# Kernel optimization log

Measured on AMD Instinct MI355X. Metric: run time of the kernel, lower is better.

Reference implementation:

```python
import jax, jax.numpy as jnp
import numpy as np

N, E, D = 50000, 800000, 128   # nodes, edges, hidden dim (in_dim == out_dim == 128)
MSG_EPS = 1e-7                 # GENConv eps added to relu(msg)
SM_EPS = 1e-16                 # PyG softmax denominator eps


def _glorotish(key, shape, fan_in):
    return jax.random.normal(key, shape, jnp.float32) * (1.0 / np.sqrt(fan_in))


def setup_inputs() -> dict:
    key = jax.random.key(0)
    ks = jax.random.split(key, 8)
    return dict(
        x=jax.random.normal(ks[0], (N, D), jnp.float32),
        edge_index=jax.random.randint(ks[1], (2, E), 0, N),
        edge_attr=jax.random.uniform(ks[2], (E, 1), jnp.float32),
        # GENConv params (bias=False internals, per PyG defaults)
        W_edge=_glorotish(ks[3], (D, 1), 1),          # lin_edge: edge_dim=1 -> D
        t=jnp.array(1.0, jnp.float32),                # learnable softmax temperature
        W1=_glorotish(ks[4], (2 * D, D), D),          # MLP: D -> 2D
        bn_gamma=jnp.ones((2 * D,), jnp.float32),     # BatchNorm1d affine
        bn_beta=jnp.zeros((2 * D,), jnp.float32),
        W2=_glorotish(ks[5], (D, 2 * D), 2 * D),      # MLP: 2D -> D
        # outer LayerNorm
        ln_gamma=jnp.ones((D,), jnp.float32),
        ln_beta=jnp.zeros((D,), jnp.float32),
        # edge_mlp: Linear(2D -> D) + GELU + LayerNorm
        We=_glorotish(ks[6], (D, 2 * D), 2 * D),
        be=jnp.zeros((D,), jnp.float32),
        ln_e_gamma=jnp.ones((D,), jnp.float32),
        ln_e_beta=jnp.zeros((D,), jnp.float32),
    )


def layer_norm(x, g, b, eps=1e-5):
    mu = x.mean(-1, keepdims=True)
    var = x.var(-1, keepdims=True)
    return (x - mu) * jax.lax.rsqrt(var + eps) * g + b


def reference(x, edge_index, edge_attr, W_edge, t, W1, bn_gamma, bn_beta, W2,
              ln_gamma, ln_beta, We, be, ln_e_gamma, ln_e_beta):
    src, dst = edge_index[0], edge_index[1]

    # --- GENConv ---
    e = edge_attr @ W_edge.T                                  # [E, D] lin_edge
    msg = jax.nn.relu(x[src] + e) + MSG_EPS                   # [E, D] message

    # per-destination scatter-softmax (per channel), temperature t
    scores = msg * t
    smax = jax.ops.segment_max(scores, dst, num_segments=N)   # [N, D]
    ex = jnp.exp(scores - smax[dst])
    denom = jax.ops.segment_sum(ex, dst, num_segments=N)      # [N, D]
    alpha = ex / (denom[dst] + SM_EPS)
    aggr = jax.ops.segment_sum(msg * alpha, dst, num_segments=N)  # [N, D]

    h = aggr + x                                              # residual (in==out dim)

    # GENConv MLP: Linear -> BatchNorm(batch stats) -> ReLU -> Linear
    h1 = h @ W1.T                                             # [N, 2D]
    mu = h1.mean(0)
    var = h1.var(0)
    h1 = (h1 - mu) * jax.lax.rsqrt(var + 1e-5) * bn_gamma + bn_beta
    h1 = jax.nn.relu(h1)
    out_conv = h1 @ W2.T                                      # [N, D]

    # --- wrapper: LayerNorm + ELU (dropout = eval identity) ---
    out_x = jax.nn.elu(layer_norm(out_conv, ln_gamma, ln_beta))

    # --- edge_mlp: gather-concat -> Linear -> GELU -> LayerNorm ---
    edge_feat = jnp.concatenate([out_x[src], out_x[dst]], axis=1)  # [E, 2D]
    out_e = layer_norm(jax.nn.gelu(edge_feat @ We.T + be, approximate=False),
                       ln_e_gamma, ln_e_beta)                 # [E, D]
    return out_x, out_e
```

## Files before the change

### kernel.cpp

```cpp
#include <hip/hip_runtime.h>
#include <math.h>


#define DIVUP(a, b) (((a) + (b) - 1) / (b))


__global__ __launch_bounds__(256) void k_hist(const int* __restrict__ dst, int* __restrict__ deg, int E) {
    int i = blockIdx.x * 256 + threadIdx.x;
    if (i < E) atomicAdd(&deg[dst[i]], 1);
}

__global__ __launch_bounds__(256) void k_scan_block(const int* __restrict__ deg, int* __restrict__ tmp,
                                                    int* __restrict__ bsum, int n) {
    __shared__ int sh[256];
    int i = blockIdx.x * 256 + threadIdx.x;
    int v = (i < n) ? deg[i] : 0;
    sh[threadIdx.x] = v;
    __syncthreads();
    #pragma unroll
    for (int off = 1; off < 256; off <<= 1) {
        int t = (threadIdx.x >= off) ? sh[threadIdx.x - off] : 0;
        __syncthreads();
        sh[threadIdx.x] += t;
        __syncthreads();
    }
    if (i < n) tmp[i] = sh[threadIdx.x];
    if (threadIdx.x == 255) bsum[blockIdx.x] = sh[255];
}

__global__ __launch_bounds__(256) void k_scan_bsum(const int* __restrict__ bsum, int* __restrict__ bsum_ex, int nb) {
    __shared__ int sh[256];
    int t = threadIdx.x;
    int v = (t < nb) ? bsum[t] : 0;
    sh[t] = v;
    __syncthreads();
    #pragma unroll
    for (int off = 1; off < 256; off <<= 1) {
        int u = (t >= off) ? sh[t - off] : 0;
        __syncthreads();
        sh[t] += u;
        __syncthreads();
    }
    bsum_ex[t] = sh[t] - v;
}

__global__ __launch_bounds__(256) void k_scan_finish(const int* __restrict__ tmp, const int* __restrict__ deg,
                                                     const int* __restrict__ bsum_ex, int* __restrict__ offs,
                                                     int* __restrict__ cursor, int n) {
    int i = blockIdx.x * 256 + threadIdx.x;
    if (i < n) {
        int ex = tmp[i] - deg[i] + bsum_ex[blockIdx.x];
        offs[i] = ex;
        cursor[i] = ex;
    }
}

__global__ __launch_bounds__(256) void k_scatter(const int* __restrict__ src, const int* __restrict__ dst,
                                                 const float* __restrict__ ea, int* __restrict__ cursor,
                                                 int* __restrict__ perm_src, float* __restrict__ perm_ea, int E) {
    int i = blockIdx.x * 256 + threadIdx.x;
    if (i < E) {
        int d = dst[i];
        int pos = atomicAdd(&cursor[d], 1);
        perm_src[pos] = src[i];
        perm_ea[pos] = ea[i];
    }
}

__global__ __launch_bounds__(128) void k_aggr_h(const int* __restrict__ offs, const int* __restrict__ deg,
                                                const int* __restrict__ perm_src, const float* __restrict__ perm_ea,
                                                const float* __restrict__ x, const float* __restrict__ W_edge,
                                                const float* __restrict__ t_ptr, float* __restrict__ h, int n) {
    int node = blockIdx.x;
    int d = threadIdx.x;
    float t = *t_ptr;
    float we = W_edge[d];
    int start = offs[node], cnt = deg[node];
    float denom = 0.f, numer = 0.f;
    for (int e = 0; e < cnt; ++e) {
        int s = perm_src[start + e];
        float ea = perm_ea[start + e];
        float m = fmaxf(x[(size_t)s * 128 + d] + ea * we, 0.f) + 1e-7f;
        float es = __expf(m * t);
        denom += es;
        numer += m * es;
    }
    h[(size_t)node * 128 + d] = numer / (denom + 1e-16f) + x[(size_t)node * 128 + d];
}

template <bool STATS>
__global__ __launch_bounds__(256) void k_gemm_nt(const float* __restrict__ A, const float* __restrict__ B,
                                                 float* __restrict__ C, int nrows,
                                                 float* __restrict__ colsum, float* __restrict__ colsq) {
    __shared__ float As[64 * 68];
    __shared__ float Bs[64 * 68];
    const int row0 = blockIdx.x * 64, col0 = blockIdx.y * 64;
    const int tid = threadIdx.x;
    const int tx = tid & 15, ty = tid >> 4;
    float acc[4][4] = {};
    for (int kc = 0; kc < 128; kc += 64) {
        #pragma unroll
        for (int q = 0; q < 4; q++) {
            int f = tid + q * 256;
            int r = f >> 4, c4 = f & 15;
            int gr = row0 + r;
            float4 av = (gr < nrows) ? *(const float4*)(A + (size_t)gr * 128 + kc + c4 * 4)
                                     : make_float4(0.f, 0.f, 0.f, 0.f);
            *(float4*)(As + r * 68 + c4 * 4) = av;
            float4 bv = *(const float4*)(B + (size_t)(col0 + r) * 128 + kc + c4 * 4);
            *(float4*)(Bs + r * 68 + c4 * 4) = bv;
        }
        __syncthreads();
        #pragma unroll
        for (int k0 = 0; k0 < 64; k0 += 4) {
            float4 a4[4], b4[4];
            #pragma unroll
            for (int i = 0; i < 4; i++) a4[i] = *(const float4*)(As + (ty * 4 + i) * 68 + k0);
            #pragma unroll
            for (int j = 0; j < 4; j++) b4[j] = *(const float4*)(Bs + (j * 16 + tx) * 68 + k0);
            #pragma unroll
            for (int i = 0; i < 4; i++)
                #pragma unroll
                for (int j = 0; j < 4; j++) {
                    acc[i][j] = fmaf(a4[i].x, b4[j].x, acc[i][j]);
                    acc[i][j] = fmaf(a4[i].y, b4[j].y, acc[i][j]);
                    acc[i][j] = fmaf(a4[i].z, b4[j].z, acc[i][j]);
                    acc[i][j] = fmaf(a4[i].w, b4[j].w, acc[i][j]);
                }
        }
        __syncthreads();
    }
    #pragma unroll
    for (int i = 0; i < 4; i++) {
        int gr = row0 + ty * 4 + i;
        if (gr < nrows) {
            #pragma unroll
            for (int j = 0; j < 4; j++) C[(size_t)gr * 256 + col0 + j * 16 + tx] = acc[i][j];
        }
    }
    if (STATS) {
        __syncthreads();
        float* redS = As;
        float* redQ = As + 1024;
        #pragma unroll
        for (int j = 0; j < 4; j++) {
            float s = 0.f, qq = 0.f;
            #pragma unroll
            for (int i = 0; i < 4; i++) {
                s += acc[i][j];
                qq += acc[i][j] * acc[i][j];
            }
            redS[(j * 16 + tx) * 16 + ty] = s;
            redQ[(j * 16 + tx) * 16 + ty] = qq;
        }
        __syncthreads();
        if (tid < 64) {
            float s = 0.f, qq = 0.f;
            #pragma unroll
            for (int u = 0; u < 16; u++) {
                s += redS[tid * 16 + u];
                qq += redQ[tid * 16 + u];
            }
            atomicAdd(&colsum[col0 + tid], s);
            atomicAdd(&colsq[col0 + tid], qq);
        }
    }
}

__global__ __launch_bounds__(256) void k_bn_finish(const float* __restrict__ colsum, const float* __restrict__ colsq,
                                                   const float* __restrict__ g, const float* __restrict__ b,
                                                   float* __restrict__ scale, float* __restrict__ shift, float invN) {
    int j = threadIdx.x;
    float mu = colsum[j] * invN;
    float var = colsq[j] * invN - mu * mu;
    float sc = g[j] * rsqrtf(var + 1e-5f);
    scale[j] = sc;
    shift[j] = b[j] - mu * sc;
}

__global__ __launch_bounds__(256) void k_gemm2(const float* __restrict__ H1, const float* __restrict__ W2,
                                               const float* __restrict__ bnscale, const float* __restrict__ bnshift,
                                               const float* __restrict__ lng, const float* __restrict__ lnb,
                                               float* __restrict__ outx, int nrows) {
    __shared__ float As[64 * 68];
    __shared__ float Bs[128 * 68];
    __shared__ float redS[64 * 16];
    __shared__ float redQ[64 * 16];
    __shared__ float rmean[64], rrstd[64];
    const int row0 = blockIdx.x * 64;
    const int tid = threadIdx.x;
    const int tx = tid & 15, ty = tid >> 4;
    float acc[4][8] = {};
    for (int kc = 0; kc < 256; kc += 64) {
        #pragma unroll
        for (int q = 0; q < 4; q++) {
            int f = tid + q * 256;
            int r = f >> 4, c4 = f & 15;
            int gr = row0 + r, kg = kc + c4 * 4;
            float4 v = (gr < nrows) ? *(const float4*)(H1 + (size_t)gr * 256 + kg)
                                    : make_float4(0.f, 0.f, 0.f, 0.f);
            float4 sc = *(const float4*)(bnscale + kg);
            float4 sh = *(const float4*)(bnshift + kg);
            v.x = fmaxf(fmaf(v.x, sc.x, sh.x), 0.f);
            v.y = fmaxf(fmaf(v.y, sc.y, sh.y), 0.f);
            v.z = fmaxf(fmaf(v.z, sc.z, sh.z), 0.f);
            v.w = fmaxf(fmaf(v.w, sc.w, sh.w), 0.f);
            *(float4*)(As + r * 68 + c4 * 4) = v;
        }
        #pragma unroll
        for (int q = 0; q < 8; q++) {
            int f = tid + q * 256;
            int r = f >> 4, c4 = f & 15;
            float4 w = *(const float4*)(W2 + (size_t)r * 256 + kc + c4 * 4);
            *(float4*)(Bs + r * 68 + c4 * 4) = w;
        }
        __syncthreads();
        #pragma unroll
        for (int k0 = 0; k0 < 64; k0 += 4) {
            float4 a4[4], b4[8];
            #pragma unroll
            for (int i = 0; i < 4; i++) a4[i] = *(const float4*)(As + (ty * 4 + i) * 68 + k0);
            #pragma unroll
            for (int j = 0; j < 8; j++) b4[j] = *(const float4*)(Bs + (j * 16 + tx) * 68 + k0);
            #pragma unroll
            for (int i = 0; i < 4; i++)
                #pragma unroll
                for (int j = 0; j < 8; j++) {
                    acc[i][j] = fmaf(a4[i].x, b4[j].x, acc[i][j]);
                    acc[i][j] = fmaf(a4[i].y, b4[j].y, acc[i][j]);
                    acc[i][j] = fmaf(a4[i].z, b4[j].z, acc[i][j]);
                    acc[i][j] = fmaf(a4[i].w, b4[j].w, acc[i][j]);
                }
        }
        __syncthreads();
    }
    #pragma unroll
    for (int i = 0; i < 4; i++) {
        float s = 0.f, qq = 0.f;
        #pragma unroll
        for (int j = 0; j < 8; j++) {
            s += acc[i][j];
            qq += acc[i][j] * acc[i][j];
        }
        redS[(ty * 4 + i) * 16 + tx] = s;
        redQ[(ty * 4 + i) * 16 + tx] = qq;
    }
    __syncthreads();
    if (tid < 64) {
        float s = 0.f, qq = 0.f;
        #pragma unroll
        for (int u = 0; u < 16; u++) {
            s += redS[tid * 16 + u];
            qq += redQ[tid * 16 + u];
        }
        float mu = s * (1.f / 128.f);
        float var = qq * (1.f / 128.f) - mu * mu;
        rmean[tid] = mu;
        rrstd[tid] = rsqrtf(var + 1e-5f);
    }
    __syncthreads();
    #pragma unroll
    for (int i = 0; i < 4; i++) {
        int lr = ty * 4 + i;
        int gr = row0 + lr;
        if (gr < nrows) {
            float mu = rmean[lr], rs = rrstd[lr];
            #pragma unroll
            for (int j = 0; j < 8; j++) {
                int col = j * 16 + tx;
                float v = (acc[i][j] - mu) * rs * lng[col] + lnb[col];
                v = v > 0.f ? v : expm1f(v);
                outx[(size_t)gr * 128 + col] = v;
            }
        }
    }
}

__global__ __launch_bounds__(256) void k_packM(const float* __restrict__ We, float* __restrict__ M) {
    int i = blockIdx.x * 256 + threadIdx.x;
    int j = i >> 7, d = i & 127;
    M[i] = (j < 128) ? We[j * 256 + d] : We[(j - 128) * 256 + 128 + d];
}

__global__ __launch_bounds__(256) void k_edge_out(const int* __restrict__ src, const int* __restrict__ dst,
                                                  const float* __restrict__ CAB, const float* __restrict__ be,
                                                  const float* __restrict__ lng, const float* __restrict__ lnb,
                                                  float* __restrict__ oute, int E) {
    int e = blockIdx.x * 4 + (threadIdx.x >> 6);
    int lane = threadIdx.x & 63;
    if (e >= E) return;
    int s = src[e], d = dst[e];
    int k = lane * 2;
    float2 va = *(const float2*)(CAB + (size_t)s * 256 + k);
    float2 vb = *(const float2*)(CAB + (size_t)d * 256 + 128 + k);
    float2 bb = *(const float2*)(be + k);
    float x0 = va.x + vb.x + bb.x;
    float x1 = va.y + vb.y + bb.y;
    const float is2 = 0.70710678118654752f;
    float g0 = 0.5f * x0 * (1.f + erff(x0 * is2));
    float g1 = 0.5f * x1 * (1.f + erff(x1 * is2));
    float s1 = g0 + g1, s2 = g0 * g0 + g1 * g1;
    #pragma unroll
    for (int off = 32; off; off >>= 1) {
        s1 += __shfl_xor(s1, off);
        s2 += __shfl_xor(s2, off);
    }
    float mu = s1 * (1.f / 128.f);
    float var = s2 * (1.f / 128.f) - mu * mu;
    float rs = rsqrtf(var + 1e-5f);
    float2 gg = *(const float2*)(lng + k);
    float2 b2 = *(const float2*)(lnb + k);
    float o0 = (g0 - mu) * rs * gg.x + b2.x;
    float o1 = (g1 - mu) * rs * gg.y + b2.y;
    *(float2*)(oute + (size_t)e * 128 + k) = make_float2(o0, o1);
}

extern "C" void kernel_launch(void* const* d_in, const int* in_sizes, int n_in,
                              void* d_out, int out_size, void* d_ws, size_t ws_size,
                              hipStream_t stream) {
    const int N = in_sizes[0] / 128;
    const int E = in_sizes[1] / 2;

    const float* x      = (const float*)d_in[0];
    const int*   ei     = (const int*)d_in[1];
    const int*   src    = ei;
    const int*   dst    = ei + E;
    const float* ea     = (const float*)d_in[2];
    const float* W_edge = (const float*)d_in[3];
    const float* t_ptr  = (const float*)d_in[4];
    const float* W1     = (const float*)d_in[5];
    const float* bng    = (const float*)d_in[6];
    const float* bnb    = (const float*)d_in[7];
    const float* W2     = (const float*)d_in[8];
    const float* lng    = (const float*)d_in[9];
    const float* lnb    = (const float*)d_in[10];
    const float* We     = (const float*)d_in[11];
    const float* be     = (const float*)d_in[12];
    const float* lneg   = (const float*)d_in[13];
    const float* lneb   = (const float*)d_in[14];

    float* out_x = (float*)d_out;
    float* out_e = out_x + (size_t)N * 128;

    float* h = (float*)d_ws;
    float* C = h + (size_t)N * 128;
    int*   perm_src = (int*)C;
    float* perm_ea  = (float*)(perm_src + E);
    int*   deg      = (int*)(perm_ea + E);
    int*   offs     = deg + N;
    int*   cursor   = offs + N;
    int*   tmp      = cursor + N;
    int*   bsum     = tmp + N;
    int*   bsum_ex  = bsum + 256;
    float* small    = C + (size_t)N * 256;
    float* colsum   = small;
    float* colsq    = small + 256;
    float* bnscale  = small + 512;
    float* bnshift  = small + 768;
    float* M        = small + 1024;

    const int EB = DIVUP(E, 256);
    const int NB = DIVUP(N, 256);
    const int GR = DIVUP(N, 64);

    hipMemsetAsync(deg, 0, (size_t)N * sizeof(int), stream);
    hipMemsetAsync(colsum, 0, 512 * sizeof(float), stream);

    k_hist<<<EB, 256, 0, stream>>>(dst, deg, E);
    k_scan_block<<<NB, 256, 0, stream>>>(deg, tmp, bsum, N);
    k_scan_bsum<<<1, 256, 0, stream>>>(bsum, bsum_ex, NB);
    k_scan_finish<<<NB, 256, 0, stream>>>(tmp, deg, bsum_ex, offs, cursor, N);
    k_scatter<<<EB, 256, 0, stream>>>(src, dst, ea, cursor, perm_src, perm_ea, E);

    k_aggr_h<<<N, 128, 0, stream>>>(offs, deg, perm_src, perm_ea, x, W_edge, t_ptr, h, N);

    k_gemm_nt<true><<<dim3(GR, 4), 256, 0, stream>>>(h, W1, C, N, colsum, colsq);
    k_bn_finish<<<1, 256, 0, stream>>>(colsum, colsq, bng, bnb, bnscale, bnshift, 1.0f / (float)N);
    k_gemm2<<<GR, 256, 0, stream>>>(C, W2, bnscale, bnshift, lng, lnb, out_x, N);

    k_packM<<<128, 256, 0, stream>>>(We, M);
    k_gemm_nt<false><<<dim3(GR, 4), 256, 0, stream>>>(out_x, M, C, N, nullptr, nullptr);
    k_edge_out<<<DIVUP(E, 4), 256, 0, stream>>>(src, dst, C, be, lneg, lneb, out_e, E);
}
```

Before: 1.041 ms.

## Move node GEMMs to fp16 MFMA and pack edge permutation into int2

Replaces the three scalar-FMA fp32 GEMMs with one templated 128x128-tile kernel that converts A to fp16 in shared memory and uses 16x16x32 f16 MFMA instructions. Weights are pre-converted to fp16 once per call, and the BN-apply, LayerNorm and ELU epilogues are folded into the template modes. The CSR permutation stores src and edge_attr together as int2, so each edge needs one load. The GEMMs are a modest share of the total compared with the edge gather and aggregation kernels, and fp16 inputs reduce precision.

Measured after the change: 909.5 us. 12.7% less time.

```diff
diff --git a/kernel.cpp b/kernel.cpp
--- a/kernel.cpp
+++ b/kernel.cpp
@@ -1,6 +1,10 @@
 #include <hip/hip_runtime.h>
 #include <math.h>
 
+typedef _Float16 f16;
+typedef _Float16 f16x4 __attribute__((ext_vector_type(4)));
+typedef _Float16 f16x8 __attribute__((ext_vector_type(8)));
+typedef float f32x4 __attribute__((ext_vector_type(4)));
 
 #define DIVUP(a, b) (((a) + (b) - 1) / (b))
 
@@ -57,18 +61,17 @@
 
 __global__ __launch_bounds__(256) void k_scatter(const int* __restrict__ src, const int* __restrict__ dst,
                                                  const float* __restrict__ ea, int* __restrict__ cursor,
-                                                 int* __restrict__ perm_src, float* __restrict__ perm_ea, int E) {
+                                                 int2* __restrict__ perm, int E) {
     int i = blockIdx.x * 256 + threadIdx.x;
     if (i < E) {
         int d = dst[i];
         int pos = atomicAdd(&cursor[d], 1);
-        perm_src[pos] = src[i];
-        perm_ea[pos] = ea[i];
+        perm[pos] = make_int2(src[i], __float_as_int(ea[i]));
     }
 }
 
 __global__ __launch_bounds__(128) void k_aggr_h(const int* __restrict__ offs, const int* __restrict__ deg,
-                                                const int* __restrict__ perm_src, const float* __restrict__ perm_ea,
+                                                const int2* __restrict__ perm,
                                                 const float* __restrict__ x, const float* __restrict__ W_edge,
                                                 const float* __restrict__ t_ptr, float* __restrict__ h, int n) {
     int node = blockIdx.x;
@@ -78,8 +81,9 @@
     int start = offs[node], cnt = deg[node];
     float denom = 0.f, numer = 0.f;
     for (int e = 0; e < cnt; ++e) {
-        int s = perm_src[start + e];
-        float ea = perm_ea[start + e];
+        int2 pe = perm[start + e];
+        int s = pe.x;
+        float ea = __int_as_float(pe.y);
         float m = fmaxf(x[(size_t)s * 128 + d] + ea * we, 0.f) + 1e-7f;
         float es = __expf(m * t);
         denom += es;
@@ -88,82 +92,167 @@
     h[(size_t)node * 128 + d] = numer / (denom + 1e-16f) + x[(size_t)node * 128 + d];
 }
 
-template <bool STATS>
-__global__ __launch_bounds__(256) void k_gemm_nt(const float* __restrict__ A, const float* __restrict__ B,
-                                                 float* __restrict__ C, int nrows,
-                                                 float* __restrict__ colsum, float* __restrict__ colsq) {
-    __shared__ float As[64 * 68];
-    __shared__ float Bs[64 * 68];
-    const int row0 = blockIdx.x * 64, col0 = blockIdx.y * 64;
+__global__ __launch_bounds__(256) void k_prep(const float* __restrict__ W1, const float* __restrict__ W2,
+                                              const float* __restrict__ We, f16* __restrict__ B1,
+                                              f16* __restrict__ B2, f16* __restrict__ BM) {
+    int i = blockIdx.x * 256 + threadIdx.x;
+    if (i < 32768) {
+        B1[i] = (f16)W1[i];
+    } else if (i < 65536) {
+        int j = i - 32768;
+        B2[j] = (f16)W2[j];
+    } else {
+        int j = i - 65536;
+        int jj = j >> 7, d = j & 127;
+        BM[j] = (f16)((jj < 128) ? We[jj * 256 + d] : We[(jj - 128) * 256 + 128 + d]);
+    }
+}
+
+template <int KTOT, int MODE>
+__global__ __launch_bounds__(256) void k_gemm(const float* __restrict__ A, const f16* __restrict__ Bg,
+                                              float* __restrict__ Cout, int nrows,
+                                              float* __restrict__ colsum, float* __restrict__ colsq,
+                                              const float* __restrict__ bnscale, const float* __restrict__ bnshift,
+                                              const float* __restrict__ lng, const float* __restrict__ lnb) {
+    __shared__ f16 As[128 * 136];
+    __shared__ f16 Bs[128 * 136];
+    __shared__ float Ssum[2][128];
+    __shared__ float Sq[2][128];
     const int tid = threadIdx.x;
-    const int tx = tid & 15, ty = tid >> 4;
-    float acc[4][4] = {};
-    for (int kc = 0; kc < 128; kc += 64) {
-        #pragma unroll
-        for (int q = 0; q < 4; q++) {
+    const int lane = tid & 63, w = tid >> 6;
+    const int m = lane & 15, quad = lane >> 4;
+    const int row0 = blockIdx.x * 128, col0 = blockIdx.y * 128;
+    const int wrow = (w & 1) * 64, wcol = (w >> 1) * 64;
+    f32x4 acc[4][4] = {};
+
+    for (int kc = 0; kc < KTOT; kc += 128) {
+        if (kc) __syncthreads();
+        #pragma unroll
+        for (int q = 0; q < 16; q++) {
             int f = tid + q * 256;
-            int r = f >> 4, c4 = f & 15;
+            int r = f >> 5, c4 = f & 31;
             int gr = row0 + r;
-            float4 av = (gr < nrows) ? *(const float4*)(A + (size_t)gr * 128 + kc + c4 * 4)
-                                     : make_float4(0.f, 0.f, 0.f, 0.f);
-            *(float4*)(As + r * 68 + c4 * 4) = av;
-            float4 bv = *(const float4*)(B + (size_t)(col0 + r) * 128 + kc + c4 * 4);
-            *(float4*)(Bs + r * 68 + c4 * 4) = bv;
-        }
-        __syncthreads();
-        #pragma unroll
-        for (int k0 = 0; k0 < 64; k0 += 4) {
-            float4 a4[4], b4[4];
-            #pragma unroll
-            for (int i = 0; i < 4; i++) a4[i] = *(const float4*)(As + (ty * 4 + i) * 68 + k0);
-            #pragma unroll
-            for (int j = 0; j < 4; j++) b4[j] = *(const float4*)(Bs + (j * 16 + tx) * 68 + k0);
+            float4 v = (gr < nrows) ? *(const float4*)(A + (size_t)gr * KTOT + kc + c4 * 4)
+                                    : make_float4(0.f, 0.f, 0.f, 0.f);
+            if (MODE == 1) {
+                float4 sc = *(const float4*)(bnscale + kc + c4 * 4);
+                float4 sh = *(const float4*)(bnshift + kc + c4 * 4);
+                v.x = fmaxf(fmaf(v.x, sc.x, sh.x), 0.f);
+                v.y = fmaxf(fmaf(v.y, sc.y, sh.y), 0.f);
+                v.z = fmaxf(fmaf(v.z, sc.z, sh.z), 0.f);
+                v.w = fmaxf(fmaf(v.w, sc.w, sh.w), 0.f);
+            }
+            f16x4 hv = {(f16)v.x, (f16)v.y, (f16)v.z, (f16)v.w};
+            *(f16x4*)(As + r * 136 + c4 * 4) = hv;
+        }
+        #pragma unroll
+        for (int q = 0; q < 8; q++) {
+            int f = tid + q * 256;
+            int r = f >> 4, k8 = f & 15;
+            *(uint4*)(Bs + r * 136 + k8 * 8) =
+                *(const uint4*)(Bg + (size_t)(col0 + r) * KTOT + kc + k8 * 8);
+        }
+        __syncthreads();
+        #pragma unroll
+        for (int k0 = 0; k0 < 128; k0 += 32) {
+            f16x8 a[4], b[4];
+            #pragma unroll
+            for (int i = 0; i < 4; i++)
+                a[i] = *(const f16x8*)(As + (wrow + i * 16 + m) * 136 + k0 + quad * 8);
+            #pragma unroll
+            for (int j = 0; j < 4; j++)
+                b[j] = *(const f16x8*)(Bs + (wcol + j * 16 + m) * 136 + k0 + quad * 8);
             #pragma unroll
             for (int i = 0; i < 4; i++)
                 #pragma unroll
-                for (int j = 0; j < 4; j++) {
-                    acc[i][j] = fmaf(a4[i].x, b4[j].x, acc[i][j]);
-                    acc[i][j] = fmaf(a4[i].y, b4[j].y, acc[i][j]);
-                    acc[i][j] = fmaf(a4[i].z, b4[j].z, acc[i][j]);
-                    acc[i][j] = fmaf(a4[i].w, b4[j].w, acc[i][j]);
-                }
-        }
-        __syncthreads();
-    }
-    #pragma unroll
-    for (int i = 0; i < 4; i++) {
-        int gr = row0 + ty * 4 + i;
-        if (gr < nrows) {
-            #pragma unroll
-            for (int j = 0; j < 4; j++) C[(size_t)gr * 256 + col0 + j * 16 + tx] = acc[i][j];
-        }
-    }
-    if (STATS) {
-        __syncthreads();
-        float* redS = As;
-        float* redQ = As + 1024;
+                for (int j = 0; j < 4; j++)
+                    acc[i][j] = __builtin_amdgcn_mfma_f32_16x16x32_f16(a[i], b[j], acc[i][j], 0, 0, 0);
+        }
+    }
+
+    if (MODE == 0 || MODE == 2) {
+        #pragma unroll
+        for (int i = 0; i < 4; i++)
+            #pragma unroll
+            for (int r = 0; r < 4; r++) {
+                int grow = row0 + wrow + i * 16 + quad * 4 + r;
+                if (grow < nrows) {
+                    #pragma unroll
+                    for (int j = 0; j < 4; j++)
+                        Cout[(size_t)grow * 256 + col0 + wcol + j * 16 + m] = acc[i][j][r];
+                }
+            }
+    }
+    if (MODE == 0) {
         #pragma unroll
         for (int j = 0; j < 4; j++) {
             float s = 0.f, qq = 0.f;
             #pragma unroll
-            for (int i = 0; i < 4; i++) {
-                s += acc[i][j];
-                qq += acc[i][j] * acc[i][j];
-            }
-            redS[(j * 16 + tx) * 16 + ty] = s;
-            redQ[(j * 16 + tx) * 16 + ty] = qq;
-        }
-        __syncthreads();
-        if (tid < 64) {
-            float s = 0.f, qq = 0.f;
-            #pragma unroll
-            for (int u = 0; u < 16; u++) {
-                s += redS[tid * 16 + u];
-                qq += redQ[tid * 16 + u];
-            }
-            atomicAdd(&colsum[col0 + tid], s);
-            atomicAdd(&colsq[col0 + tid], qq);
-        }
+            for (int i = 0; i < 4; i++)
+                #pragma unroll
+                for (int r = 0; r < 4; r++) {
+                    float v = acc[i][j][r];
+                    s += v;
+                    qq += v * v;
+                }
+            s += __shfl_xor(s, 16); s += __shfl_xor(s, 32);
+            qq += __shfl_xor(qq, 16); qq += __shfl_xor(qq, 32);
+            if (lane < 16) {
+                atomicAdd(&colsum[col0 + wcol + j * 16 + lane], s);
+                atomicAdd(&colsq[col0 + wcol + j * 16 + lane], qq);
+            }
+        }
+    }
+    if (MODE == 1) {
+        const int cw = w >> 1;
+        #pragma unroll
+        for (int i = 0; i < 4; i++)
+            #pragma unroll
+            for (int r = 0; r < 4; r++) {
+                float s = 0.f, qq = 0.f;
+                #pragma unroll
+                for (int j = 0; j < 4; j++) {
+                    float v = acc[i][j][r];
+                    s += v;
+                    qq += v * v;
+                }
+                s += __shfl_xor(s, 1); s += __shfl_xor(s, 2);
+                s += __shfl_xor(s, 4); s += __shfl_xor(s, 8);
+                qq += __shfl_xor(qq, 1); qq += __shfl_xor(qq, 2);
+                qq += __shfl_xor(qq, 4); qq += __shfl_xor(qq, 8);
+                if (m == 0) {
+                    int lrow = wrow + i * 16 + quad * 4 + r;
+                    Ssum[cw][lrow] = s;
+                    Sq[cw][lrow] = qq;
+                }
+            }
+        __syncthreads();
+        float lg[4], lb[4];
+        #pragma unroll
+        for (int j = 0; j < 4; j++) {
+            lg[j] = lng[wcol + j * 16 + m];
+            lb[j] = lnb[wcol + j * 16 + m];
+        }
+        #pragma unroll
+        for (int i = 0; i < 4; i++)
+            #pragma unroll
+            for (int r = 0; r < 4; r++) {
+                int lrow = wrow + i * 16 + quad * 4 + r;
+                int grow = row0 + lrow;
+                if (grow < nrows) {
+                    float S = Ssum[0][lrow] + Ssum[1][lrow];
+                    float Q = Sq[0][lrow] + Sq[1][lrow];
+                    float mu = S * (1.f / 128.f);
+                    float var = Q * (1.f / 128.f) - mu * mu;
+                    float rs = rsqrtf(var + 1e-5f);
+                    #pragma unroll
+                    for (int j = 0; j < 4; j++) {
+                        float v = (acc[i][j][r] - mu) * rs * lg[j] + lb[j];
+                        v = v > 0.f ? v : expm1f(v);
+                        Cout[(size_t)grow * 128 + wcol + j * 16 + m] = v;
+                    }
+                }
+            }
     }
 }
 
@@ -176,110 +265,6 @@
     float sc = g[j] * rsqrtf(var + 1e-5f);
     scale[j] = sc;
     shift[j] = b[j] - mu * sc;
-}
-
-__global__ __launch_bounds__(256) void k_gemm2(const float* __restrict__ H1, const float* __restrict__ W2,
-                                               const float* __restrict__ bnscale, const float* __restrict__ bnshift,
-                                               const float* __restrict__ lng, const float* __restrict__ lnb,
-                                               float* __restrict__ outx, int nrows) {
-    __shared__ float As[64 * 68];
-    __shared__ float Bs[128 * 68];
-    __shared__ float redS[64 * 16];
-    __shared__ float redQ[64 * 16];
-    __shared__ float rmean[64], rrstd[64];
-    const int row0 = blockIdx.x * 64;
-    const int tid = threadIdx.x;
-    const int tx = tid & 15, ty = tid >> 4;
-    float acc[4][8] = {};
-    for (int kc = 0; kc < 256; kc += 64) {
-        #pragma unroll
-        for (int q = 0; q < 4; q++) {
-            int f = tid + q * 256;
-            int r = f >> 4, c4 = f & 15;
-            int gr = row0 + r, kg = kc + c4 * 4;
-            float4 v = (gr < nrows) ? *(const float4*)(H1 + (size_t)gr * 256 + kg)
-                                    : make_float4(0.f, 0.f, 0.f, 0.f);
-            float4 sc = *(const float4*)(bnscale + kg);
-            float4 sh = *(const float4*)(bnshift + kg);
-            v.x = fmaxf(fmaf(v.x, sc.x, sh.x), 0.f);
-            v.y = fmaxf(fmaf(v.y, sc.y, sh.y), 0.f);
-            v.z = fmaxf(fmaf(v.z, sc.z, sh.z), 0.f);
-            v.w = fmaxf(fmaf(v.w, sc.w, sh.w), 0.f);
-            *(float4*)(As + r * 68 + c4 * 4) = v;
-        }
-        #pragma unroll
-        for (int q = 0; q < 8; q++) {
-            int f = tid + q * 256;
-            int r = f >> 4, c4 = f & 15;
-            float4 w = *(const float4*)(W2 + (size_t)r * 256 + kc + c4 * 4);
-            *(float4*)(Bs + r * 68 + c4 * 4) = w;
-        }
-        __syncthreads();
-        #pragma unroll
-        for (int k0 = 0; k0 < 64; k0 += 4) {
-            float4 a4[4], b4[8];
-            #pragma unroll
-            for (int i = 0; i < 4; i++) a4[i] = *(const float4*)(As + (ty * 4 + i) * 68 + k0);
-            #pragma unroll
-            for (int j = 0; j < 8; j++) b4[j] = *(const float4*)(Bs + (j * 16 + tx) * 68 + k0);
-            #pragma unroll
-            for (int i = 0; i < 4; i++)
-                #pragma unroll
-                for (int j = 0; j < 8; j++) {
-                    acc[i][j] = fmaf(a4[i].x, b4[j].x, acc[i][j]);
-                    acc[i][j] = fmaf(a4[i].y, b4[j].y, acc[i][j]);
-                    acc[i][j] = fmaf(a4[i].z, b4[j].z, acc[i][j]);
-                    acc[i][j] = fmaf(a4[i].w, b4[j].w, acc[i][j]);
-                }
-        }
-        __syncthreads();
-    }
-    #pragma unroll
-    for (int i = 0; i < 4; i++) {
-        float s = 0.f, qq = 0.f;
-        #pragma unroll
-        for (int j = 0; j < 8; j++) {
-            s += acc[i][j];
-            qq += acc[i][j] * acc[i][j];
-        }
-        redS[(ty * 4 + i) * 16 + tx] = s;
-        redQ[(ty * 4 + i) * 16 + tx] = qq;
-    }
-    __syncthreads();
-    if (tid < 64) {
-        float s = 0.f, qq = 0.f;
-        #pragma unroll
-        for (int u = 0; u < 16; u++) {
-            s += redS[tid * 16 + u];
-            qq += redQ[tid * 16 + u];
-        }
-        float mu = s * (1.f / 128.f);
-        float var = qq * (1.f / 128.f) - mu * mu;
-        rmean[tid] = mu;
-        rrstd[tid] = rsqrtf(var + 1e-5f);
-    }
-    __syncthreads();
-    #pragma unroll
-    for (int i = 0; i < 4; i++) {
-        int lr = ty * 4 + i;
-        int gr = row0 + lr;
-        if (gr < nrows) {
-            float mu = rmean[lr], rs = rrstd[lr];
-            #pragma unroll
-            for (int j = 0; j < 8; j++) {
-                int col = j * 16 + tx;
-                float v = (acc[i][j] - mu) * rs * lng[col] + lnb[col];
-                v = v > 0.f ? v : expm1f(v);
-                outx[(size_t)gr * 128 + col] = v;
-            }
-        }
-    }
-}
-
-__global__ __launch_bounds__(256) void k_packM(const float* __restrict__ We, float* __restrict__ M) {
-    int i = blockIdx.x * 256 + threadIdx.x;
-    int j = i >> 7, d = i & 127;
-    M[i] = (j < 128) ? We[j * 256 + d] : We[(j - 128) * 256 + 128 + d];
 }
 
 __global__ __launch_bounds__(256) void k_edge_out(const int* __restrict__ src, const int* __restrict__ dst,
@@ -344,9 +329,8 @@
 
     float* h = (float*)d_ws;
     float* C = h + (size_t)N * 128;
-    int*   perm_src = (int*)C;
-    float* perm_ea  = (float*)(perm_src + E);
-    int*   deg      = (int*)(perm_ea + E);
+    int2*  perm     = (int2*)C;
+    int*   deg      = (int*)(perm + E);
     int*   offs     = deg + N;
     int*   cursor   = offs + N;
     int*   tmp      = cursor + N;
@@ -357,28 +341,34 @@
     float* colsq    = small + 256;
     float* bnscale  = small + 512;
     float* bnshift  = small + 768;
-    float* M        = small + 1024;
+    f16*   B1f16    = (f16*)(small + 1024);
+    f16*   B2f16    = B1f16 + 32768;
+    f16*   BMf16    = B2f16 + 32768;
 
     const int EB = DIVUP(E, 256);
     const int NB = DIVUP(N, 256);
-    const int GR = DIVUP(N, 64);
+    const int GR = DIVUP(N, 128);
 
     hipMemsetAsync(deg, 0, (size_t)N * sizeof(int), stream);
     hipMemsetAsync(colsum, 0, 512 * sizeof(float), stream);
+
+    k_prep<<<384, 256, 0, stream>>>(W1, W2, We, B1f16, B2f16, BMf16);
 
     k_hist<<<EB, 256, 0, stream>>>(dst, deg, E);
     k_scan_block<<<NB, 256, 0, stream>>>(deg, tmp, bsum, N);
     k_scan_bsum<<<1, 256, 0, stream>>>(bsum, bsum_ex, NB);
     k_scan_finish<<<NB, 256, 0, stream>>>(tmp, deg, bsum_ex, offs, cursor, N);
-    k_scatter<<<EB, 256, 0, stream>>>(src, dst, ea, cursor, perm_src, perm_ea, E);
-
-    k_aggr_h<<<N, 128, 0, stream>>>(offs, deg, perm_src, perm_ea, x, W_edge, t_ptr, h, N);
-
-    k_gemm_nt<true><<<dim3(GR, 4), 256, 0, stream>>>(h, W1, C, N, colsum, colsq);
+    k_scatter<<<EB, 256, 0, stream>>>(src, dst, ea, cursor, perm, E);
+
+    k_aggr_h<<<N, 128, 0, stream>>>(offs, deg, perm, x, W_edge, t_ptr, h, N);
+
+    k_gemm<128, 0><<<dim3(GR, 2), 256, 0, stream>>>(h, B1f16, C, N, colsum, colsq,
+                                                    nullptr, nullptr, nullptr, nullptr);
     k_bn_finish<<<1, 256, 0, stream>>>(colsum, colsq, bng, bnb, bnscale, bnshift, 1.0f / (float)N);
-    k_gemm2<<<GR, 256, 0, stream>>>(C, W2, bnscale, bnshift, lng, lnb, out_x, N);
-
-    k_packM<<<128, 256, 0, stream>>>(We, M);
-    k_gemm_nt<false><<<dim3(GR, 4), 256, 0, stream>>>(out_x, M, C, N, nullptr, nullptr);
+    k_gemm<256, 1><<<dim3(GR, 1), 256, 0, stream>>>(C, B2f16, out_x, N, nullptr, nullptr,
+                                                    bnscale, bnshift, lng, lnb);
+
+    k_gemm<128, 2><<<dim3(GR, 2), 256, 0, stream>>>(out_x, BMf16, C, N, nullptr, nullptr,
+                                                    nullptr, nullptr, nullptr, nullptr);
     k_edge_out<<<DIVUP(E, 4), 256, 0, stream>>>(src, dst, C, be, lneg, lneb, out_e, E);
 }
```
